# Optimization experiments

Hardware: AMD Instinct MI355X
Metric: run time of the kernel (lower is better)

Reference implementation:

```python
import jax, jax.numpy as jnp
import numpy as np
import math

N = 8192
F_DIM = 128
ALPHA_SLOPE = 0.2  # LeakyReLU negative slope from __init__ alpha


def setup_inputs() -> dict:
    key = jax.random.key(0)
    k1, k2, k3, k4, k5 = jax.random.split(key, 5)
    inp = jax.random.normal(k1, (N, F_DIM), dtype=jnp.float32)
    adj = (jax.random.uniform(k2, (N, N)) < 0.02).astype(jnp.float32)
    adj = adj.at[jnp.arange(N), jnp.arange(N)].set(1.0)
    h0 = jax.random.normal(k3, (N, F_DIM), dtype=jnp.float32)
    W = jax.random.normal(k4, (F_DIM, F_DIM), dtype=jnp.float32) * (1.414 * math.sqrt(6.0 / (2 * F_DIM)))
    a = jax.random.normal(k5, (2 * F_DIM, 1), dtype=jnp.float32) * (1.414 * math.sqrt(6.0 / (2 * F_DIM + 1)))
    return {"inp": inp, "adj": adj, "h0": h0, "W": W, "a": a,
            "lamda": 0.5, "alpha_mix": 0.1, "l": 1}


def reference(inp, adj, h0, W, a, lamda, alpha_mix, l):
    # h = inp @ W  -> (N, F)
    h = inp @ W
    # score(i,j) = leakyrelu([h_i, h_j] @ a) = leakyrelu(h_i@a1 + h_j@a2)
    # avoids materializing the O(N^2 * 2F) a_input tensor of the original
    f1 = h @ a[:F_DIM, 0]   # (N,)
    f2 = h @ a[F_DIM:, 0]   # (N,)
    e = jax.nn.leaky_relu(f1[:, None] + f2[None, :], negative_slope=ALPHA_SLOPE)  # (N, N)
    e = jnp.where(adj > 0, e, jnp.float32(-1e12))
    attention = jax.nn.softmax(e, axis=1)
    # dropout skipped (inference / training=False)
    hi = attention @ inp                      # (N, F) -- note: aggregates inp, not h
    support = (1.0 - alpha_mix) * hi + alpha_mix * h0
    theta = min(1.0, math.log(lamda / l + 1.0))
    output = theta * (support @ W) + (1.0 - theta) * support + inp
    return output
```

## Files before the change

### kernel.cpp

```cpp
#include <hip/hip_runtime.h>
#include <math.h>

#define N 8192
#define F 128
#define SLOPE 0.2f
#define SEGCAP 96
#define FB 512
#define RPB 4

typedef float f4v __attribute__((ext_vector_type(4)));

__device__ __forceinline__ float lrelu(float x) { return x > 0.0f ? x : SLOPE * x; }

__device__ __forceinline__ int mbcnt64(unsigned long long m) {
    return __builtin_amdgcn_mbcnt_hi((unsigned)(m >> 32),
                                     __builtin_amdgcn_mbcnt_lo((unsigned)m, 0u));
}

__device__ __forceinline__ unsigned bf16pair(float a, float b) {
    unsigned ua = __builtin_bit_cast(unsigned, a);
    unsigned ub = __builtin_bit_cast(unsigned, b);
    ua = (ua + 0x7FFFu + ((ua >> 16) & 1u)) >> 16;
    ub = (ub + 0x7FFFu + ((ub >> 16) & 1u)) >> 16;
    return ua | (ub << 16);
}
__device__ __forceinline__ float bflo(unsigned u) {
    return __builtin_bit_cast(float, u << 16);
}
__device__ __forceinline__ float bfhi(unsigned u) {
    return __builtin_bit_cast(float, u & 0xFFFF0000u);
}

__global__ __launch_bounds__(256, 8) void k_main(const float* __restrict__ adj,
                                                 const float* __restrict__ inp,
                                                 const float* __restrict__ W,
                                                 const float* __restrict__ a,
                                                 float* __restrict__ f1,
                                                 float* __restrict__ f2,
                                                 unsigned* __restrict__ inpb,
                                                 int* __restrict__ nzidx,
                                                 int* __restrict__ nzcnt) {
    const int bid = blockIdx.x;
    const int t = threadIdx.x;
    const int wv = t >> 6;
    const int lane = t & 63;

    if (bid < FB) {
        __shared__ float Wa_l[2 * F];
        {
            const int k = t & 127;
            const int half = t >> 7;
            const f4v* wr = reinterpret_cast<const f4v*>(W + k * F);
            const f4v* av = reinterpret_cast<const f4v*>(a + half * F);
            float s = 0.f;
            #pragma unroll
            for (int q = 0; q < 32; ++q) {
                const f4v w = wr[q], aa = av[q];
                s += (w[0] * aa[0] + w[1] * aa[1]) + (w[2] * aa[2] + w[3] * aa[3]);
            }
            Wa_l[t] = s;
        }
        __syncthreads();
        const float w1a = Wa_l[2 * lane], w1b = Wa_l[2 * lane + 1];
        const float w2a = Wa_l[F + 2 * lane], w2b = Wa_l[F + 2 * lane + 1];
        #pragma unroll
        for (int r = 0; r < 4; ++r) {
            const int i = bid * 16 + wv * 4 + r;
            const float2 xv = *reinterpret_cast<const float2*>(inp + (size_t)i * F + 2 * lane);
            float v1 = xv.x * w1a + xv.y * w1b;
            float v2 = xv.x * w2a + xv.y * w2b;
            #pragma unroll
            for (int off = 32; off; off >>= 1) {
                v1 += __shfl_xor(v1, off);
                v2 += __shfl_xor(v2, off);
            }
            if (lane == 0) { f1[i] = v1; f2[i] = v2; }
            inpb[i * 64 + lane] = bf16pair(xv.x, xv.y);
        }
    } else {
        __shared__ int s_seg[4][SEGCAP];
        const int row = bid - FB;
        const float* base = adj + (size_t)row * N + wv * 2048 + lane * 4;
        f4v v[8];
        #pragma unroll
        for (int u = 0; u < 8; ++u)
            v[u] = *reinterpret_cast<const f4v*>(base + u * 256);

        int cnt = 0;
        #pragma unroll
        for (int u = 0; u < 8; ++u) {
            const int col0 = wv * 2048 + u * 256 + lane * 4;
            #pragma unroll
            for (int c = 0; c < 4; ++c) {
                const bool nz = v[u][c] > 0.f;
                const unsigned long long m = __ballot(nz);
                const int pos = mbcnt64(m);
                int p = cnt + pos;
                if (p > SEGCAP - 1) p = SEGCAP - 1;
                if (nz) s_seg[wv][p] = col0 + c;
                cnt += (int)__popcll(m);
            }
        }
        const int M = cnt > SEGCAP ? SEGCAP : cnt;
        int* seg = nzidx + ((size_t)row * 4 + wv) * SEGCAP;
        for (int t2 = lane; t2 < M; t2 += 64) seg[t2] = s_seg[wv][t2];
        if (lane == 0) nzcnt[row * 4 + wv] = M;
    }
}

__global__ __launch_bounds__(256, 4) void k_agg(const int* __restrict__ nzidx,
                                                const int* __restrict__ nzcnt,
                                                const unsigned* __restrict__ inpb,
                                                const float* __restrict__ inp,
                                                const float* __restrict__ h0,
                                                const float* __restrict__ W,
                                                const float* __restrict__ f1,
                                                const float* __restrict__ f2,
                                                const float* __restrict__ lamda_p,
                                                const float* __restrict__ alpha_p,
                                                const int* __restrict__ l_p,
                                                float* __restrict__ out) {
    const int r0 = blockIdx.x * RPB;
    const int t = threadIdx.x;
    const int lane = t & 63;
    const int wv = t >> 6;
    const int i = r0 + wv;

    __shared__ int   s_j[RPB][400];
    __shared__ float s_w[RPB][400];
    __shared__ float s_sup[RPB][F];
    __shared__ float s_dot[RPB][F];

    const float f1i = f1[i];

    int cnts[4], jA[4], jB[4];
    float sA[4], sB[4];
    float mx = -1e30f;
    #pragma unroll
    for (int s = 0; s < 4; ++s) {
        cnts[s] = nzcnt[i * 4 + s];
        const int* seg = nzidx + ((size_t)i * 4 + s) * SEGCAP;
        jA[s] = (lane < cnts[s]) ? seg[lane] : -1;
        jB[s] = (64 + lane < cnts[s]) ? seg[64 + lane] : -1;
        sA[s] = (jA[s] >= 0) ? lrelu(f1i + f2[jA[s]]) : -1e30f;
        sB[s] = (jB[s] >= 0) ? lrelu(f1i + f2[jB[s]]) : -1e30f;
        mx = fmaxf(mx, fmaxf(sA[s], sB[s]));
    }
    #pragma unroll
    for (int off = 32; off; off >>= 1) mx = fmaxf(mx, __shfl_xor(mx, off));

    int total = 0;
    float wlane = 0.f;
    #pragma unroll
    for (int s = 0; s < 4; ++s) {
        float w1 = 0.f, w2 = 0.f;
        if (jA[s] >= 0) {
            w1 = __expf(sA[s] - mx);
            s_j[wv][total + lane] = jA[s];
            s_w[wv][total + lane] = w1;
        }
        if (jB[s] >= 0) {
            w2 = __expf(sB[s] - mx);
            s_j[wv][total + 64 + lane] = jB[s];
            s_w[wv][total + 64 + lane] = w2;
        }
        wlane += w1 + w2;
        total += cnts[s];
    }
    if (lane < 8) { s_j[wv][total + lane] = 0; s_w[wv][total + lane] = 0.f; }
    float wsum = wlane;
    #pragma unroll
    for (int off = 32; off; off >>= 1) wsum += __shfl_xor(wsum, off);

    float acc_e = 0.f, acc_o = 0.f;
    for (int e = 0; e < total; e += 8) {
        const int4 jv0 = *reinterpret_cast<const int4*>(&s_j[wv][e]);
        const int4 jv1 = *reinterpret_cast<const int4*>(&s_j[wv][e + 4]);
        const f4v  wq0 = *reinterpret_cast<const f4v*>(&s_w[wv][e]);
        const f4v  wq1 = *reinterpret_cast<const f4v*>(&s_w[wv][e + 4]);
        const unsigned a0 = inpb[(size_t)jv0.x * 64 + lane];
        const unsigned a1 = inpb[(size_t)jv0.y * 64 + lane];
        const unsigned a2 = inpb[(size_t)jv0.z * 64 + lane];
        const unsigned a3 = inpb[(size_t)jv0.w * 64 + lane];
        const unsigned a4 = inpb[(size_t)jv1.x * 64 + lane];
        const unsigned a5 = inpb[(size_t)jv1.y * 64 + lane];
        const unsigned a6 = inpb[(size_t)jv1.z * 64 + lane];
        const unsigned a7 = inpb[(size_t)jv1.w * 64 + lane];
        acc_e = fmaf(wq0[0], bflo(a0), acc_e); acc_o = fmaf(wq0[0], bfhi(a0), acc_o);
        acc_e = fmaf(wq0[1], bflo(a1), acc_e); acc_o = fmaf(wq0[1], bfhi(a1), acc_o);
        acc_e = fmaf(wq0[2], bflo(a2), acc_e); acc_o = fmaf(wq0[2], bfhi(a2), acc_o);
        acc_e = fmaf(wq0[3], bflo(a3), acc_e); acc_o = fmaf(wq0[3], bfhi(a3), acc_o);
        acc_e = fmaf(wq1[0], bflo(a4), acc_e); acc_o = fmaf(wq1[0], bfhi(a4), acc_o);
        acc_e = fmaf(wq1[1], bflo(a5), acc_e); acc_o = fmaf(wq1[1], bfhi(a5), acc_o);
        acc_e = fmaf(wq1[2], bflo(a6), acc_e); acc_o = fmaf(wq1[2], bfhi(a6), acc_o);
        acc_e = fmaf(wq1[3], bflo(a7), acc_e); acc_o = fmaf(wq1[3], bfhi(a7), acc_o);
    }

    const float inv = 1.0f / wsum;
    const float alpha = *alpha_p;
    const float2 hv = *reinterpret_cast<const float2*>(h0 + (size_t)i * F + 2 * lane);
    const float sup_e = (1.0f - alpha) * (acc_e * inv) + alpha * hv.x;
    const float sup_o = (1.0f - alpha) * (acc_o * inv) + alpha * hv.y;
    s_sup[wv][2 * lane]     = sup_e;
    s_sup[wv][2 * lane + 1] = sup_o;
    __syncthreads();

    const int c = t & 127;
    const int h = t >> 7;
    float d0 = 0.f, d1 = 0.f, d2 = 0.f, d3 = 0.f;
    const int k0 = 64 * h;
    #pragma unroll 4
    for (int k = k0; k < k0 + 64; ++k) {
        const float wk = W[k * F + c];
        d0 = fmaf(s_sup[0][k], wk, d0);
        d1 = fmaf(s_sup[1][k], wk, d1);
        d2 = fmaf(s_sup[2][k], wk, d2);
        d3 = fmaf(s_sup[3][k], wk, d3);
    }
    if (h == 0) {
        s_dot[0][c] = d0; s_dot[1][c] = d1; s_dot[2][c] = d2; s_dot[3][c] = d3;
    }
    __syncthreads();
    if (h == 1) {
        const float lam = *lamda_p;
        const float th = fminf(1.0f, logf(lam / (float)(*l_p) + 1.0f));
        const float dr[4] = { d0 + s_dot[0][c], d1 + s_dot[1][c],
                              d2 + s_dot[2][c], d3 + s_dot[3][c] };
        #pragma unroll
        for (int r = 0; r < RPB; ++r) {
            const size_t o = (size_t)(r0 + r) * F + c;
            out[o] = th * dr[r] + (1.0f - th) * s_sup[r][c] + inp[o];
        }
    }
}

extern "C" void kernel_launch(void* const* d_in, const int* in_sizes, int n_in,
                              void* d_out, int out_size, void* d_ws, size_t ws_size,
                              hipStream_t stream) {
    const float* inp   = (const float*)d_in[0];
    const float* adj   = (const float*)d_in[1];
    const float* h0    = (const float*)d_in[2];
    const float* W     = (const float*)d_in[3];
    const float* a     = (const float*)d_in[4];
    const float* lamda = (const float*)d_in[5];
    const float* alpha = (const float*)d_in[6];
    const int*   l     = (const int*)d_in[7];
    float* out = (float*)d_out;

    float* ws = (float*)d_ws;
    float*    f1    = ws;
    float*    f2    = ws + N;
    int*      nzcnt = (int*)(ws + 2 * N);
    int*      nzidx = (int*)(ws + 2 * N + 4 * N);
    unsigned* inpb  = (unsigned*)(ws + 6 * N + 4 * N * SEGCAP);

    hipLaunchKernelGGL(k_main, dim3(FB + N), dim3(256), 0, stream,
                       adj, inp, W, a, f1, f2, inpb, nzidx, nzcnt);
    hipLaunchKernelGGL(k_agg, dim3(N / RPB), dim3(256), 0, stream,
                       nzidx, nzcnt, inpb, inp, h0, W, f1, f2, lamda, alpha, l, out);
}
```

Measured before the change: 90.63 us.

## Fuse adjacency compaction into aggregation kernel, one wave per row scan

```diff
diff --git a/kernel.cpp b/kernel.cpp
--- a/kernel.cpp
+++ b/kernel.cpp
@@ -4,9 +4,9 @@
 #define N 8192
 #define F 128
 #define SLOPE 0.2f
-#define SEGCAP 96
+#define CAP 320
+#define NSLOT 5
 #define FB 512
-#define RPB 4
 
 typedef float f4v __attribute__((ext_vector_type(4)));
 
@@ -31,153 +31,144 @@
     return __builtin_bit_cast(float, u & 0xFFFF0000u);
 }
 
-__global__ __launch_bounds__(256, 8) void k_main(const float* __restrict__ adj,
-                                                 const float* __restrict__ inp,
-                                                 const float* __restrict__ W,
-                                                 const float* __restrict__ a,
-                                                 float* __restrict__ f1,
-                                                 float* __restrict__ f2,
-                                                 unsigned* __restrict__ inpb,
-                                                 int* __restrict__ nzidx,
-                                                 int* __restrict__ nzcnt) {
-    const int bid = blockIdx.x;
+__global__ __launch_bounds__(256) void k_pre(const float* __restrict__ inp,
+                                             const float* __restrict__ W,
+                                             const float* __restrict__ a,
+                                             float* __restrict__ f1,
+                                             float* __restrict__ f2,
+                                             unsigned* __restrict__ inpb) {
     const int t = threadIdx.x;
     const int wv = t >> 6;
     const int lane = t & 63;
-
-    if (bid < FB) {
-        __shared__ float Wa_l[2 * F];
-        {
-            const int k = t & 127;
-            const int half = t >> 7;
-            const f4v* wr = reinterpret_cast<const f4v*>(W + k * F);
-            const f4v* av = reinterpret_cast<const f4v*>(a + half * F);
-            float s = 0.f;
-            #pragma unroll
-            for (int q = 0; q < 32; ++q) {
-                const f4v w = wr[q], aa = av[q];
-                s += (w[0] * aa[0] + w[1] * aa[1]) + (w[2] * aa[2] + w[3] * aa[3]);
-            }
-            Wa_l[t] = s;
-        }
-        __syncthreads();
-        const float w1a = Wa_l[2 * lane], w1b = Wa_l[2 * lane + 1];
-        const float w2a = Wa_l[F + 2 * lane], w2b = Wa_l[F + 2 * lane + 1];
+    __shared__ float Wa_l[2 * F];
+    {
+        const int k = t & 127;
+        const int half = t >> 7;
+        const f4v* wr = reinterpret_cast<const f4v*>(W + k * F);
+        const f4v* av = reinterpret_cast<const f4v*>(a + half * F);
+        float s = 0.f;
         #pragma unroll
-        for (int r = 0; r < 4; ++r) {
-            const int i = bid * 16 + wv * 4 + r;
-            const float2 xv = *reinterpret_cast<const float2*>(inp + (size_t)i * F + 2 * lane);
-            float v1 = xv.x * w1a + xv.y * w1b;
-            float v2 = xv.x * w2a + xv.y * w2b;
-            #pragma unroll
-            for (int off = 32; off; off >>= 1) {
-                v1 += __shfl_xor(v1, off);
-                v2 += __shfl_xor(v2, off);
-            }
-            if (lane == 0) { f1[i] = v1; f2[i] = v2; }
-            inpb[i * 64 + lane] = bf16pair(xv.x, xv.y);
-        }
-    } else {
-        __shared__ int s_seg[4][SEGCAP];
-        const int row = bid - FB;
-        const float* base = adj + (size_t)row * N + wv * 2048 + lane * 4;
-        f4v v[8];
+        for (int q = 0; q < 32; ++q) {
+            const f4v w = wr[q], aa = av[q];
+            s += (w[0] * aa[0] + w[1] * aa[1]) + (w[2] * aa[2] + w[3] * aa[3]);
+        }
+        Wa_l[t] = s;
+    }
+    __syncthreads();
+    const float w1a = Wa_l[2 * lane], w1b = Wa_l[2 * lane + 1];
+    const float w2a = Wa_l[F + 2 * lane], w2b = Wa_l[F + 2 * lane + 1];
+    #pragma unroll
+    for (int r = 0; r < 4; ++r) {
+        const int i = blockIdx.x * 16 + wv * 4 + r;
+        const float2 xv = *reinterpret_cast<const float2*>(inp + (size_t)i * F + 2 * lane);
+        float v1 = xv.x * w1a + xv.y * w1b;
+        float v2 = xv.x * w2a + xv.y * w2b;
         #pragma unroll
-        for (int u = 0; u < 8; ++u)
-            v[u] = *reinterpret_cast<const f4v*>(base + u * 256);
-
-        int cnt = 0;
-        #pragma unroll
-        for (int u = 0; u < 8; ++u) {
-            const int col0 = wv * 2048 + u * 256 + lane * 4;
-            #pragma unroll
-            for (int c = 0; c < 4; ++c) {
-                const bool nz = v[u][c] > 0.f;
-                const unsigned long long m = __ballot(nz);
-                const int pos = mbcnt64(m);
-                int p = cnt + pos;
-                if (p > SEGCAP - 1) p = SEGCAP - 1;
-                if (nz) s_seg[wv][p] = col0 + c;
-                cnt += (int)__popcll(m);
-            }
-        }
-        const int M = cnt > SEGCAP ? SEGCAP : cnt;
-        int* seg = nzidx + ((size_t)row * 4 + wv) * SEGCAP;
-        for (int t2 = lane; t2 < M; t2 += 64) seg[t2] = s_seg[wv][t2];
-        if (lane == 0) nzcnt[row * 4 + wv] = M;
-    }
-}
-
-__global__ __launch_bounds__(256, 4) void k_agg(const int* __restrict__ nzidx,
-                                                const int* __restrict__ nzcnt,
-                                                const unsigned* __restrict__ inpb,
-                                                const float* __restrict__ inp,
-                                                const float* __restrict__ h0,
-                                                const float* __restrict__ W,
-                                                const float* __restrict__ f1,
-                                                const float* __restrict__ f2,
-                                                const float* __restrict__ lamda_p,
-                                                const float* __restrict__ alpha_p,
-                                                const int* __restrict__ l_p,
-                                                float* __restrict__ out) {
-    const int r0 = blockIdx.x * RPB;
+        for (int off = 32; off; off >>= 1) {
+            v1 += __shfl_xor(v1, off);
+            v2 += __shfl_xor(v2, off);
+        }
+        if (lane == 0) { f1[i] = v1; f2[i] = v2; }
+        inpb[i * 64 + lane] = bf16pair(xv.x, xv.y);
+    }
+}
+
+__global__ __launch_bounds__(256, 4) void k_fused(const float* __restrict__ adj,
+                                                  const unsigned* __restrict__ inpb,
+                                                  const float* __restrict__ inp,
+                                                  const float* __restrict__ h0,
+                                                  const float* __restrict__ W,
+                                                  const float* __restrict__ f1,
+                                                  const float* __restrict__ f2,
+                                                  const float* __restrict__ lamda_p,
+                                                  const float* __restrict__ alpha_p,
+                                                  const int* __restrict__ l_p,
+                                                  float* __restrict__ out) {
     const int t = threadIdx.x;
+    const int w = t >> 6;
     const int lane = t & 63;
-    const int wv = t >> 6;
-    const int i = r0 + wv;
-
-    __shared__ int   s_j[RPB][400];
-    __shared__ float s_w[RPB][400];
-    __shared__ float s_sup[RPB][F];
-    __shared__ float s_dot[RPB][F];
+    const int rowblk = (blockIdx.x & 7) * 256 + (blockIdx.x >> 3);
+    const int i = rowblk * 4 + w;
+
+    __shared__ int   s_j[4][CAP + 8];
+    __shared__ float s_w[4][CAP + 8];
+    __shared__ float s_sup[4][F];
+    __shared__ float s_dot[4][F];
 
     const float f1i = f1[i];
-
-    int cnts[4], jA[4], jB[4];
-    float sA[4], sB[4];
+    const float* rowp = adj + (size_t)i * N + lane * 4;
+
+    f4v b0[8], b1[8];
+    int cnt = 0;
+
+#define LOADCH(DST, CH)                                                        \
+    _Pragma("unroll")                                                          \
+    for (int u = 0; u < 8; ++u)                                                \
+        DST[u] = *reinterpret_cast<const f4v*>(rowp + (CH) * 2048 + u * 256);
+
+#define PROCCH(SRC, CH)                                                        \
+    _Pragma("unroll")                                                          \
+    for (int u = 0; u < 8; ++u) {                                              \
+        const int col0 = (CH) * 2048 + u * 256 + lane * 4;                     \
+        _Pragma("unroll")                                                      \
+        for (int c = 0; c < 4; ++c) {                                          \
+            const bool nz = SRC[u][c] > 0.f;                                   \
+            const unsigned long long m = __ballot(nz);                         \
+            const int pos = mbcnt64(m);                                        \
+            int p = cnt + pos;                                                 \
+            if (p > CAP - 1) p = CAP - 1;                                      \
+            if (nz) s_j[w][p] = col0 + c;                                      \
+            cnt += (int)__popcll(m);                                           \
+        }                                                                      \
+    }
+
+    LOADCH(b0, 0)
+    LOADCH(b1, 1)
+    PROCCH(b0, 0)
+    LOADCH(b0, 2)
+    PROCCH(b1, 1)
+    LOADCH(b1, 3)
+    PROCCH(b0, 2)
+    PROCCH(b1, 3)
+#undef LOADCH
+#undef PROCCH
+
+    const int M = cnt > CAP ? CAP : cnt;
+
+    int   jj[NSLOT];
+    float ss[NSLOT];
     float mx = -1e30f;
     #pragma unroll
-    for (int s = 0; s < 4; ++s) {
-        cnts[s] = nzcnt[i * 4 + s];
-        const int* seg = nzidx + ((size_t)i * 4 + s) * SEGCAP;
-        jA[s] = (lane < cnts[s]) ? seg[lane] : -1;
-        jB[s] = (64 + lane < cnts[s]) ? seg[64 + lane] : -1;
-        sA[s] = (jA[s] >= 0) ? lrelu(f1i + f2[jA[s]]) : -1e30f;
-        sB[s] = (jB[s] >= 0) ? lrelu(f1i + f2[jB[s]]) : -1e30f;
-        mx = fmaxf(mx, fmaxf(sA[s], sB[s]));
+    for (int s = 0; s < NSLOT; ++s) {
+        const int e = s * 64 + lane;
+        jj[s] = (e < M) ? s_j[w][e] : -1;
+        ss[s] = (jj[s] >= 0) ? lrelu(f1i + f2[jj[s]]) : -1e30f;
+        mx = fmaxf(mx, ss[s]);
     }
     #pragma unroll
     for (int off = 32; off; off >>= 1) mx = fmaxf(mx, __shfl_xor(mx, off));
 
-    int total = 0;
-    float wlane = 0.f;
-    #pragma unroll
-    for (int s = 0; s < 4; ++s) {
-        float w1 = 0.f, w2 = 0.f;
-        if (jA[s] >= 0) {
-            w1 = __expf(sA[s] - mx);
-            s_j[wv][total + lane] = jA[s];
-            s_w[wv][total + lane] = w1;
-        }
-        if (jB[s] >= 0) {
-            w2 = __expf(sB[s] - mx);
-            s_j[wv][total + 64 + lane] = jB[s];
-            s_w[wv][total + 64 + lane] = w2;
-        }
-        wlane += w1 + w2;
-        total += cnts[s];
-    }
-    if (lane < 8) { s_j[wv][total + lane] = 0; s_w[wv][total + lane] = 0.f; }
-    float wsum = wlane;
-    #pragma unroll
-    for (int off = 32; off; off >>= 1) wsum += __shfl_xor(wsum, off);
+    float wl = 0.f;
+    #pragma unroll
+    for (int s = 0; s < NSLOT; ++s) {
+        if (jj[s] >= 0) {
+            const float ww = __expf(ss[s] - mx);
+            s_w[w][s * 64 + lane] = ww;
+            wl += ww;
+        }
+    }
+    if (lane < 8) { s_j[w][M + lane] = 0; s_w[w][M + lane] = 0.f; }
+    #pragma unroll
+    for (int off = 32; off; off >>= 1) wl += __shfl_xor(wl, off);
+    const float wsum = wl;
 
     float acc_e = 0.f, acc_o = 0.f;
-    for (int e = 0; e < total; e += 8) {
-        const int4 jv0 = *reinterpret_cast<const int4*>(&s_j[wv][e]);
-        const int4 jv1 = *reinterpret_cast<const int4*>(&s_j[wv][e + 4]);
-        const f4v  wq0 = *reinterpret_cast<const f4v*>(&s_w[wv][e]);
-        const f4v  wq1 = *reinterpret_cast<const f4v*>(&s_w[wv][e + 4]);
+    const int MP = (M + 7) & ~7;
+    for (int e = 0; e < MP; e += 8) {
+        const int4 jv0 = *reinterpret_cast<const int4*>(&s_j[w][e]);
+        const int4 jv1 = *reinterpret_cast<const int4*>(&s_j[w][e + 4]);
+        const f4v  wq0 = *reinterpret_cast<const f4v*>(&s_w[w][e]);
+        const f4v  wq1 = *reinterpret_cast<const f4v*>(&s_w[w][e + 4]);
         const unsigned a0 = inpb[(size_t)jv0.x * 64 + lane];
         const unsigned a1 = inpb[(size_t)jv0.y * 64 + lane];
         const unsigned a2 = inpb[(size_t)jv0.z * 64 + lane];
@@ -199,10 +190,8 @@
     const float inv = 1.0f / wsum;
     const float alpha = *alpha_p;
     const float2 hv = *reinterpret_cast<const float2*>(h0 + (size_t)i * F + 2 * lane);
-    const float sup_e = (1.0f - alpha) * (acc_e * inv) + alpha * hv.x;
-    const float sup_o = (1.0f - alpha) * (acc_o * inv) + alpha * hv.y;
-    s_sup[wv][2 * lane]     = sup_e;
-    s_sup[wv][2 * lane + 1] = sup_o;
+    s_sup[w][2 * lane]     = (1.0f - alpha) * (acc_e * inv) + alpha * hv.x;
+    s_sup[w][2 * lane + 1] = (1.0f - alpha) * (acc_o * inv) + alpha * hv.y;
     __syncthreads();
 
     const int c = t & 127;
@@ -227,8 +216,8 @@
         const float dr[4] = { d0 + s_dot[0][c], d1 + s_dot[1][c],
                               d2 + s_dot[2][c], d3 + s_dot[3][c] };
         #pragma unroll
-        for (int r = 0; r < RPB; ++r) {
-            const size_t o = (size_t)(r0 + r) * F + c;
+        for (int r = 0; r < 4; ++r) {
+            const size_t o = (size_t)(rowblk * 4 + r) * F + c;
             out[o] = th * dr[r] + (1.0f - th) * s_sup[r][c] + inp[o];
         }
     }
@@ -248,14 +237,12 @@
     float* out = (float*)d_out;
 
     float* ws = (float*)d_ws;
-    float*    f1    = ws;
-    float*    f2    = ws + N;
-    int*      nzcnt = (int*)(ws + 2 * N);
-    int*      nzidx = (int*)(ws + 2 * N + 4 * N);
-    unsigned* inpb  = (unsigned*)(ws + 6 * N + 4 * N * SEGCAP);
-
-    hipLaunchKernelGGL(k_main, dim3(FB + N), dim3(256), 0, stream,
-                       adj, inp, W, a, f1, f2, inpb, nzidx, nzcnt);
-    hipLaunchKernelGGL(k_agg, dim3(N / RPB), dim3(256), 0, stream,
-                       nzidx, nzcnt, inpb, inp, h0, W, f1, f2, lamda, alpha, l, out);
-}
+    float*    f1   = ws;
+    float*    f2   = ws + N;
+    unsigned* inpb = (unsigned*)(ws + 2 * N);
+
+    hipLaunchKernelGGL(k_pre, dim3(FB), dim3(256), 0, stream,
+                       inp, W, a, f1, f2, inpb);
+    hipLaunchKernelGGL(k_fused, dim3(N / 4), dim3(256), 0, stream,
+                       adj, inpb, inp, h0, W, f1, f2, lamda, alpha, l, out);
+}
```

Result: no change. 91.24 us (+0.7%).
